# Optimization experiments

Measured on AMD Instinct MI355X. Metric: run time of the kernel, lower is better.

The kernel has to match this reference:

```python
import jax, jax.numpy as jnp
import numpy as np
import math

N = 10000      # atoms
E = 320000     # neighbor pairs (edges)
NELEM = 3      # species one-hot size
NRAD = 8       # radial channels per component
NB = 8         # bessel basis size
ZETA = 4       # max angular moment
RC = 5.0       # radial cutoff
S = 4          # species embedding size (species_layer_sizes[-1])
NCOMP = (ZETA + 2) * NRAD   # 2-body slice + (ZETA+1) angular slices = 48
FEAT = NCOMP * S            # 192

# multinomial expansion of (r_i . r_j)^l : lxlylz powers and l!/(lx!ly!lz!) norms
_TERMS = []
for l in range(ZETA + 1):
    pw, nm = [], []
    for a in range(l + 1):
        for b in range(l + 1 - a):
            c = l - a - b
            pw.append((a, b, c))
            nm.append(math.factorial(l) / (math.factorial(a) * math.factorial(b) * math.factorial(c)))
    _TERMS.append((np.array(pw, dtype=np.float32), np.array(nm, dtype=np.float32)))


def _silu(x):
    return x * jax.nn.sigmoid(x)


def setup_inputs() -> dict:
    key = jax.random.key(0)
    ks = jax.random.split(key, 12)
    rij = (jax.random.uniform(ks[0], (E, 3), minval=-1.0, maxval=1.0) * (RC / math.sqrt(3.0))).astype(jnp.float32)
    first_atom = jax.random.randint(ks[1], (E,), 0, N, dtype=jnp.int32)
    second_atom = jax.random.randint(ks[2], (E,), 0, N, dtype=jnp.int32)
    species_idx = jax.random.randint(ks[3], (N,), 0, NELEM, dtype=jnp.int32)
    w = lambda k, s: (jax.random.normal(k, s) * 0.1).astype(jnp.float32)
    z = lambda s: jnp.zeros(s, jnp.float32)
    return dict(
        rij=rij, species_idx=species_idx, first_atom=first_atom, second_atom=second_atom,
        Wr1=w(ks[4], (NB, 64)), br1=z((64,)),
        Wr2=w(ks[5], (64, NCOMP)), br2=z((NCOMP,)),
        Ws1=w(ks[6], (NELEM, 16)), bs1=z((16,)),
        Ws2=w(ks[7], (16, S)), bs2=z((S,)),
        Wa1=w(ks[8], (FEAT, 64)), ba1=z((64,)),
        Wa2=w(ks[9], (64, 64)), ba2=z((64,)),
        Wa3=w(ks[10], (64, 1)), ba3=z((1,)),
    )


def reference(rij, species_idx, first_atom, second_atom,
              Wr1, br1, Wr2, br2, Ws1, bs1, Ws2, bs2,
              Wa1, ba1, Wa2, ba2, Wa3, ba3):
    d = jnp.sqrt(jnp.sum(rij * rij, axis=-1) + 1e-12)            # [E]
    rhat = rij / d[:, None]                                       # [E,3]
    fc = jnp.where(d < RC, 0.5 * (jnp.cos(np.pi * d / RC) + 1.0), 0.0)
    n = jnp.arange(1, NB + 1, dtype=rij.dtype)
    bes = jnp.sqrt(2.0 / RC) * jnp.sin(n[None, :] * np.pi * d[:, None] / RC) / d[:, None]  # [E,NB]
    # learned radial functions, all components at once, smoothed by cutoff
    R = _silu(_silu(bes @ Wr1 + br1) @ Wr2 + br2) * fc[:, None]   # [E, NCOMP]
    # species encoder -> per-atom embedding, gathered on neighbor atom j
    onehot = jax.nn.one_hot(species_idx, NELEM, dtype=rij.dtype)  # [N,NELEM]
    semb = jnp.tanh(onehot @ Ws1 + bs1) @ Ws2 + bs2               # [N,S]
    sj = semb[second_atom]                                        # [E,S]
    # 2-body feature
    feats = [jax.ops.segment_sum(R[:, :NRAD, None] * sj[:, None, :], first_atom, num_segments=N)]  # [N,NRAD,S]
    off = NRAD
    for l in range(ZETA + 1):
        pw, nm = _TERMS[l]
        comps = jnp.prod(rhat[:, None, :] ** jnp.asarray(pw)[None, :, :], axis=-1)  # [E,C_l]
        Rl = R[:, off:off + NRAD]
        off += NRAD
        edge = Rl[:, :, None, None] * comps[:, None, :, None] * sj[:, None, None, :]  # [E,NRAD,C_l,S]
        A = jax.ops.segment_sum(edge, first_atom, num_segments=N)                     # [N,NRAD,C_l,S]
        feats.append(jnp.einsum('nrcs,c->nrs', A * A, jnp.asarray(nm)))               # [N,NRAD,S]
    feat = jnp.concatenate(feats, axis=1).reshape(N, -1)          # [N, FEAT]
    h = _silu(feat @ Wa1 + ba1)
    h = _silu(h @ Wa2 + ba2)
    return (h @ Wa3 + ba3)[:, 0]                                  # per-atom energies [N]
```

## Files before the change

kernel.cpp:

```cpp
#include <hip/hip_runtime.h>
#include <math.h>

#define NATOMS 10000
#define NEDGES 320000
#define CAP    64
#define RC_F 5.0f
#define PI_F 3.14159265358979323846f

#define NK   16384
#define TROW 48
#define HINV_F ((float)(NK - 1) / RC_F)

#define WS_SEMB   0
#define WS_CNT    16
#define WS_SD     440096
#define WS_TAB    8200096

__device__ __constant__ int   d_PWA[35] = {0, 0,0,1, 0,0,0,1,1,2, 0,0,0,0,1,1,1,2,2,3, 0,0,0,0,0,1,1,1,1,2,2,2,3,3,4};
__device__ __constant__ int   d_PWB[35] = {0, 0,1,0, 0,1,2,0,1,0, 0,1,2,3,0,1,2,0,1,0, 0,1,2,3,4,0,1,2,3,0,1,2,0,1,0};
__device__ __constant__ int   d_PWC[35] = {0, 1,0,0, 2,1,0,1,0,0, 3,2,1,0,2,1,0,1,0,0, 4,3,2,1,0,3,2,1,0,2,1,0,1,0,0};
__device__ __constant__ float d_NM[35]  = {1.f, 1.f,1.f,1.f, 1.f,2.f,1.f,2.f,2.f,1.f,
                                           1.f,3.f,3.f,1.f,3.f,6.f,3.f,3.f,3.f,1.f,
                                           1.f,4.f,6.f,4.f,1.f,4.f,12.f,12.f,4.f,6.f,12.f,6.f,4.f,4.f,1.f};
__device__ __constant__ int   d_LBLK[35]= {0, 1,1,1, 2,2,2,2,2,2, 3,3,3,3,3,3,3,3,3,3, 4,4,4,4,4,4,4,4,4,4,4,4,4,4,4};
__device__ __constant__ int   d_L6[6]   = {0,1,4,10,20,35};

__device__ __forceinline__ float siluf(float x) { return x / (1.0f + __expf(-x)); }

__device__ __forceinline__ float2 f2fma(float2 a, float2 b, float2 c) {
  return make_float2(fmaf(a.x, b.x, c.x), fmaf(a.y, b.y, c.y));
}

__device__ __forceinline__ float psel(float x, int p) {
  float x2 = x * x;
  float r = 1.0f;
  r = (p == 1) ? x : r;
  r = (p == 2) ? x2 : r;
  r = (p == 3) ? x2 * x : r;
  r = (p == 4) ? x2 * x2 : r;
  return r;
}

__global__ __launch_bounds__(256) void k_pre(
    const float* __restrict__ Wr1, const float* __restrict__ br1,
    const float* __restrict__ Wr2, const float* __restrict__ br2,
    const float* __restrict__ Ws1, const float* __restrict__ bs1,
    const float* __restrict__ Ws2, const float* __restrict__ bs2,
    float* __restrict__ ws)
{
  int gt = blockIdx.x * 256 + threadIdx.x;

  if (gt < NATOMS) ((int4*)(ws + WS_CNT))[gt] = make_int4(0, 0, 0, 0);
  if (gt < 12) {
    int t = gt >> 2, s = gt & 3;
    float acc = bs2[s];
    for (int j = 0; j < 16; j++) acc += tanhf(Ws1[t * 16 + j] + bs1[j]) * Ws2[j * 4 + s];
    ws[WS_SEMB + gt] = acc;
  }

  int sl = gt % 12;
  int k  = gt / 12;
  float dk = (float)k * (RC_F / (float)(NK - 1));
  float d = fmaxf(dk, 1e-6f);
  float invd = 1.0f / d;
  float theta = (PI_F / RC_F) * d;
  float s1 = sinf(theta), c1 = cosf(theta);
  float fc = (d < RC_F) ? 0.5f * (c1 + 1.0f) : 0.0f;
  float bes[8];
  {
    float sq = sqrtf(2.0f / RC_F) * invd;
    float twoc = 2.0f * c1;
    float sp = 0.0f, sc = s1;
    #pragma unroll
    for (int q = 0; q < 8; q++) {
      bes[q] = sq * sc;
      float sn = twoc * sc - sp;
      sp = sc; sc = sn;
    }
  }
  float h1[64];
  #pragma unroll
  for (int j4 = 0; j4 < 16; j4++) {
    float2 a01 = *(const float2*)&br1[j4 * 4];
    float2 a23 = *(const float2*)&br1[j4 * 4 + 2];
    #pragma unroll
    for (int q = 0; q < 8; q++) {
      float2 b2 = make_float2(bes[q], bes[q]);
      a01 = f2fma(b2, *(const float2*)&Wr1[q * 64 + j4 * 4],     a01);
      a23 = f2fma(b2, *(const float2*)&Wr1[q * 64 + j4 * 4 + 2], a23);
    }
    h1[j4 * 4 + 0] = siluf(a01.x);
    h1[j4 * 4 + 1] = siluf(a01.y);
    h1[j4 * 4 + 2] = siluf(a23.x);
    h1[j4 * 4 + 3] = siluf(a23.y);
  }
  int j0 = sl * 4;
  float2 a01 = *(const float2*)&br2[j0];
  float2 a23 = *(const float2*)&br2[j0 + 2];
  for (int q = 0; q < 64; q++) {
    float2 h2 = make_float2(h1[q], h1[q]);
    a01 = f2fma(h2, *(const float2*)&Wr2[q * 48 + j0],     a01);
    a23 = f2fma(h2, *(const float2*)&Wr2[q * 48 + j0 + 2], a23);
  }
  *(float4*)(ws + WS_TAB + (size_t)k * TROW + j0) =
      make_float4(siluf(a01.x) * fc, siluf(a01.y) * fc,
                  siluf(a23.x) * fc, siluf(a23.y) * fc);
}

__global__ __launch_bounds__(256) void k_scatter(
    const float* __restrict__ rij,
    const int* __restrict__ first_atom, const int* __restrict__ second_atom,
    const int* __restrict__ species, float* __restrict__ ws)
{
  int e = blockIdx.x * 256 + threadIdx.x;
  int* cnt = (int*)(ws + WS_CNT);
  int a = first_atom[e];
  int t = species[second_atom[e]];
  int pos = atomicAdd(&cnt[a * 4 + t], 1);
  float x = rij[e * 3 + 0], y = rij[e * 3 + 1], z = rij[e * 3 + 2];
  float d = sqrtf(x * x + y * y + z * z + 1e-12f);
  float invd = 1.0f / d;
  if (pos < CAP)
    ((float4*)(ws + WS_SD))[(size_t)a * (3 * CAP) + t * CAP + pos] =
        make_float4(x * invd, y * invd, z * invd, d);
}

__global__ __launch_bounds__(128) void k_atom(
    const float* __restrict__ ws,
    const float* __restrict__ Wa1, const float* __restrict__ ba1,
    const float* __restrict__ Wa2, const float* __restrict__ ba2,
    const float* __restrict__ Wa3, const float* __restrict__ ba3,
    float* __restrict__ out)
{
  __shared__ __align__(16) float sScr[2][1120];
  int tid = threadIdx.x;
  int lane = tid & 63, wv = tid >> 6;
  int a = blockIdx.x * 2 + wv;
  float* sStage = &sScr[wv][0];
  float* sG     = &sScr[wv][0];
  float* sFeat  = &sScr[wv][864];
  float* sH     = &sScr[wv][1056];

  const float4* sd4 = (const float4*)(ws + WS_SD);
  const float* tab = ws + WS_TAB;

  const int c = lane;
  bool isc = (c < 35);
  int pa = 0, pb = 0, pcw = 0, lb = 0;
  if (isc) { pa = d_PWA[c]; pb = d_PWB[c]; pcw = d_PWC[c]; lb = d_LBLK[c]; }
  int rdir = lane - 35;
  bool isd = (rdir >= 0) && (rdir < 8);
  int rl = lane >> 4, fl = lane & 15;
  int s = lane & 3;
  float se0 = ws[WS_SEMB + s], se1 = ws[WS_SEMB + 4 + s], se2 = ws[WS_SEMB + 8 + s];

  int4 cv = ((const int4*)(ws + WS_CNT))[a];
  int c0n = cv.x > CAP ? CAP : cv.x;
  int c1n = cv.y > CAP ? CAP : cv.y;
  int c2n = cv.z > CAP ? CAP : cv.z;

  float2 g2[3][4];
  #pragma unroll
  for (int t2 = 0; t2 < 3; t2++)
    #pragma unroll
    for (int r = 0; r < 4; r++) g2[t2][r] = make_float2(0.f, 0.f);
  float g0[3] = {0.0f, 0.0f, 0.0f};

#define CORE(T) {                                                             \
    const float* rb = sStage + j * 52;                                        \
    if (isc) {                                                                \
      float4 rh = *(const float4*)(rb + 48);                                  \
      float comp = psel(rh.x, pa) * psel(rh.y, pb) * psel(rh.z, pcw);         \
      float2 c2v = make_float2(comp, comp);                                   \
      const float2* r2 = (const float2*)(rb + 8 + 8 * lb);                    \
      g2[T][0] = f2fma(c2v, r2[0], g2[T][0]);                                 \
      g2[T][1] = f2fma(c2v, r2[1], g2[T][1]);                                 \
      g2[T][2] = f2fma(c2v, r2[2], g2[T][2]);                                 \
      g2[T][3] = f2fma(c2v, r2[3], g2[T][3]);                                 \
    } else if (isd) {                                                         \
      g0[T] += rb[rdir];                                                      \
    }                                                                         \
  }

#define RUNT(T, CT) {                                                         \
    const float4* rbase = sd4 + (size_t)a * (3 * CAP) + (T) * CAP;            \
    for (int cb = 0; cb < (CT); cb += 16) {                                   \
      int m = (CT) - cb; if (m > 16) m = 16;                                  \
      float4 ed = rbase[cb + ((lane < m) ? lane : (m - 1))];                  \
      float fi = ed.w * HINV_F;                                               \
      int ii = (int)fi;                                                       \
      ii = (ii > NK - 2) ? (NK - 2) : ii;                                     \
      float w = fi - (float)ii;                                               \
      int rowb = ii * TROW;                                                   \
      int R = (m + 3) >> 2;                                                   \
      for (int r = 0; r < R; r++) {                                           \
        int sl = r * 4 + rl;                                                  \
        float w_s = __shfl(w, sl, 64);                                        \
        int   rb_ = __shfl(rowb, sl, 64);                                     \
        float sx = __shfl(ed.x, sl, 64), sy = __shfl(ed.y, sl, 64);           \
        float sz = __shfl(ed.z, sl, 64);                                      \
        if (fl < 12) {                                                        \
          const float* tp = tab + rb_ + fl * 4;                               \
          float4 t0 = *(const float4*)(tp);                                   \
          float4 t1 = *(const float4*)(tp + TROW);                            \
          float4 v;                                                           \
          v.x = fmaf(w_s, t1.x - t0.x, t0.x);                                 \
          v.y = fmaf(w_s, t1.y - t0.y, t0.y);                                 \
          v.z = fmaf(w_s, t1.z - t0.z, t0.z);                                 \
          v.w = fmaf(w_s, t1.w - t0.w, t0.w);                                 \
          *(float4*)(sStage + sl * 52 + fl * 4) = v;                          \
        } else if (fl == 12) {                                                \
          *(float4*)(sStage + sl * 52 + 48) = make_float4(sx, sy, sz, 0.0f);  \
        }                                                                     \
      }                                                                       \
      for (int j = 0; j < m; j++) CORE(T)                                     \
    }                                                                         \
  }

  RUNT(0, c0n)
  RUNT(1, c1n)
  RUNT(2, c2n)
#undef RUNT
#undef CORE

  if (isc) {
    #pragma unroll
    for (int t2 = 0; t2 < 3; t2++)
      #pragma unroll
      for (int r = 0; r < 8; r++) {
        float gval = (r & 1) ? g2[t2][r >> 1].y : g2[t2][r >> 1].x;
        sG[(t2 * 8 + r) * 36 + c] = gval;
      }
  } else if (isd) {
    #pragma unroll
    for (int t2 = 0; t2 < 3; t2++) sG[(t2 * 8 + rdir) * 36 + 35] = g0[t2];
  }

  float fout[3];
  #pragma unroll
  for (int u = 0; u < 3; u++) {
    int f = lane + 64 * u;
    int blk = f >> 5, rr = (f >> 2) & 7;
    float acc;
    if (blk == 0) {
      acc = se0 * sG[(0 + rr) * 36 + 35] + se1 * sG[(8 + rr) * 36 + 35] + se2 * sG[(16 + rr) * 36 + 35];
    } else {
      int cc0 = d_L6[blk - 1], cc1 = d_L6[blk];
      acc = 0.0f;
      for (int cc = cc0; cc < cc1; cc++) {
        float A = se0 * sG[(0 + rr) * 36 + cc] + se1 * sG[(8 + rr) * 36 + cc] + se2 * sG[(16 + rr) * 36 + cc];
        acc += d_NM[cc] * A * A;
      }
    }
    fout[u] = acc;
  }
  #pragma unroll
  for (int u = 0; u < 3; u++) sFeat[lane + 64 * u] = fout[u];

  {
    float a0_ = 0.f, a1_ = 0.f, a2_ = 0.f, a3_ = 0.f;
    for (int k4 = 0; k4 < 48; k4++) {
      float4 f4 = *(const float4*)(sFeat + k4 * 4);
      const float* wp = Wa1 + (k4 * 4) * 64 + lane;
      a0_ += f4.x * wp[0];
      a1_ += f4.y * wp[64];
      a2_ += f4.z * wp[128];
      a3_ += f4.w * wp[192];
    }
    sH[lane] = siluf(a0_ + a1_ + a2_ + a3_ + ba1[lane]);
  }

  {
    float a0_ = 0.f, a1_ = 0.f, a2_ = 0.f, a3_ = 0.f;
    for (int k4 = 0; k4 < 16; k4++) {
      float4 h4 = *(const float4*)(sH + k4 * 4);
      const float* wp = Wa2 + (k4 * 4) * 64 + lane;
      a0_ += h4.x * wp[0];
      a1_ += h4.y * wp[64];
      a2_ += h4.z * wp[128];
      a3_ += h4.w * wp[192];
    }
    float h2 = siluf(a0_ + a1_ + a2_ + a3_ + ba2[lane]);
    float pr = h2 * Wa3[lane];
    #pragma unroll
    for (int off = 32; off > 0; off >>= 1) pr += __shfl_down(pr, off, 64);
    if (lane == 0) out[a] = pr + ba3[0];
  }
}

extern "C" void kernel_launch(void* const* d_in, const int* in_sizes, int n_in,
                              void* d_out, int out_size, void* d_ws, size_t ws_size,
                              hipStream_t stream)
{
  const float* rij         = (const float*)d_in[0];
  const int*   species     = (const int*)  d_in[1];
  const int*   first_atom  = (const int*)  d_in[2];
  const int*   second_atom = (const int*)  d_in[3];
  const float* Wr1 = (const float*)d_in[4];
  const float* br1 = (const float*)d_in[5];
  const float* Wr2 = (const float*)d_in[6];
  const float* br2 = (const float*)d_in[7];
  const float* Ws1 = (const float*)d_in[8];
  const float* bs1 = (const float*)d_in[9];
  const float* Ws2 = (const float*)d_in[10];
  const float* bs2 = (const float*)d_in[11];
  const float* Wa1 = (const float*)d_in[12];
  const float* ba1 = (const float*)d_in[13];
  const float* Wa2 = (const float*)d_in[14];
  const float* ba2 = (const float*)d_in[15];
  const float* Wa3 = (const float*)d_in[16];
  const float* ba3 = (const float*)d_in[17];
  float* ws  = (float*)d_ws;
  float* out = (float*)d_out;

  k_pre<<<(NK * 12) / 256, 256, 0, stream>>>(Wr1, br1, Wr2, br2, Ws1, bs1, Ws2, bs2, ws);
  k_scatter<<<NEDGES / 256, 256, 0, stream>>>(rij, first_atom, second_atom, species, ws);
  k_atom<<<NATOMS / 2, 128, 0, stream>>>(ws, Wa1, ba1, Wa2, ba2, Wa3, ba3, out);
}
```

Baseline: 172.6 us.

## Read radial table directly per lane instead of staging edges through LDS

Drops the cooperative staging step, where 16-edge chunks were interpolated into shared memory via shuffles and then consumed. Each lane now loads each edge's record (a broadcast load), interpolates the radial table slice for its own angular block from global or cache, and accumulates directly. This removes shuffles, LDS writes and reads, and the two-phase structure. In exchange, every lane issues redundant global loads of the same table rows (35 lanes reading overlapping 8-float slices), and the edge loop becomes sequential with a dependent load per edge.

```diff
diff --git a/kernel.cpp b/kernel.cpp
--- a/kernel.cpp
+++ b/kernel.cpp
@@ -136,7 +136,6 @@
   int tid = threadIdx.x;
   int lane = tid & 63, wv = tid >> 6;
   int a = blockIdx.x * 2 + wv;
-  float* sStage = &sScr[wv][0];
   float* sG     = &sScr[wv][0];
   float* sFeat  = &sScr[wv][864];
   float* sH     = &sScr[wv][1056];
@@ -146,11 +145,10 @@
 
   const int c = lane;
   bool isc = (c < 35);
-  int pa = 0, pb = 0, pcw = 0, lb = 0;
-  if (isc) { pa = d_PWA[c]; pb = d_PWB[c]; pcw = d_PWC[c]; lb = d_LBLK[c]; }
+  int pa = 0, pb = 0, pcw = 0, my8 = 8;
+  if (isc) { pa = d_PWA[c]; pb = d_PWB[c]; pcw = d_PWC[c]; my8 = 8 + 8 * d_LBLK[c]; }
   int rdir = lane - 35;
   bool isd = (rdir >= 0) && (rdir < 8);
-  int rl = lane >> 4, fl = lane & 15;
   int s = lane & 3;
   float se0 = ws[WS_SEMB + s], se1 = ws[WS_SEMB + 4 + s], se2 = ws[WS_SEMB + 8 + s];
 
@@ -166,54 +164,40 @@
     for (int r = 0; r < 4; r++) g2[t2][r] = make_float2(0.f, 0.f);
   float g0[3] = {0.0f, 0.0f, 0.0f};
 
-#define CORE(T) {                                                             \
-    const float* rb = sStage + j * 52;                                        \
-    if (isc) {                                                                \
-      float4 rh = *(const float4*)(rb + 48);                                  \
-      float comp = psel(rh.x, pa) * psel(rh.y, pb) * psel(rh.z, pcw);         \
-      float2 c2v = make_float2(comp, comp);                                   \
-      const float2* r2 = (const float2*)(rb + 8 + 8 * lb);                    \
-      g2[T][0] = f2fma(c2v, r2[0], g2[T][0]);                                 \
-      g2[T][1] = f2fma(c2v, r2[1], g2[T][1]);                                 \
-      g2[T][2] = f2fma(c2v, r2[2], g2[T][2]);                                 \
-      g2[T][3] = f2fma(c2v, r2[3], g2[T][3]);                                 \
-    } else if (isd) {                                                         \
-      g0[T] += rb[rdir];                                                      \
-    }                                                                         \
-  }
-
 #define RUNT(T, CT) {                                                         \
     const float4* rbase = sd4 + (size_t)a * (3 * CAP) + (T) * CAP;            \
-    for (int cb = 0; cb < (CT); cb += 16) {                                   \
-      int m = (CT) - cb; if (m > 16) m = 16;                                  \
-      float4 ed = rbase[cb + ((lane < m) ? lane : (m - 1))];                  \
+    _Pragma("unroll 4")                                                       \
+    for (int j = 0; j < (CT); j++) {                                          \
+      float4 ed = rbase[j];                                                   \
       float fi = ed.w * HINV_F;                                               \
       int ii = (int)fi;                                                       \
       ii = (ii > NK - 2) ? (NK - 2) : ii;                                     \
       float w = fi - (float)ii;                                               \
-      int rowb = ii * TROW;                                                   \
-      int R = (m + 3) >> 2;                                                   \
-      for (int r = 0; r < R; r++) {                                           \
-        int sl = r * 4 + rl;                                                  \
-        float w_s = __shfl(w, sl, 64);                                        \
-        int   rb_ = __shfl(rowb, sl, 64);                                     \
-        float sx = __shfl(ed.x, sl, 64), sy = __shfl(ed.y, sl, 64);           \
-        float sz = __shfl(ed.z, sl, 64);                                      \
-        if (fl < 12) {                                                        \
-          const float* tp = tab + rb_ + fl * 4;                               \
-          float4 t0 = *(const float4*)(tp);                                   \
-          float4 t1 = *(const float4*)(tp + TROW);                            \
-          float4 v;                                                           \
-          v.x = fmaf(w_s, t1.x - t0.x, t0.x);                                 \
-          v.y = fmaf(w_s, t1.y - t0.y, t0.y);                                 \
-          v.z = fmaf(w_s, t1.z - t0.z, t0.z);                                 \
-          v.w = fmaf(w_s, t1.w - t0.w, t0.w);                                 \
-          *(float4*)(sStage + sl * 52 + fl * 4) = v;                          \
-        } else if (fl == 12) {                                                \
-          *(float4*)(sStage + sl * 52 + 48) = make_float4(sx, sy, sz, 0.0f);  \
-        }                                                                     \
+      const float* tp0 = tab + ii * TROW;                                     \
+      if (isc) {                                                              \
+        const float* ta = tp0 + my8;                                          \
+        float4 t0a = *(const float4*)(ta);                                    \
+        float4 t0b = *(const float4*)(ta + 4);                                \
+        float4 t1a = *(const float4*)(ta + TROW);                             \
+        float4 t1b = *(const float4*)(ta + TROW + 4);                         \
+        float comp = psel(ed.x, pa) * psel(ed.y, pb) * psel(ed.z, pcw);       \
+        float2 c2v = make_float2(comp, comp);                                 \
+        float2 v0 = make_float2(fmaf(w, t1a.x - t0a.x, t0a.x),                \
+                                fmaf(w, t1a.y - t0a.y, t0a.y));               \
+        float2 v1 = make_float2(fmaf(w, t1a.z - t0a.z, t0a.z),                \
+                                fmaf(w, t1a.w - t0a.w, t0a.w));               \
+        float2 v2 = make_float2(fmaf(w, t1b.x - t0b.x, t0b.x),                \
+                                fmaf(w, t1b.y - t0b.y, t0b.y));               \
+        float2 v3 = make_float2(fmaf(w, t1b.z - t0b.z, t0b.z),                \
+                                fmaf(w, t1b.w - t0b.w, t0b.w));               \
+        g2[T][0] = f2fma(c2v, v0, g2[T][0]);                                  \
+        g2[T][1] = f2fma(c2v, v1, g2[T][1]);                                  \
+        g2[T][2] = f2fma(c2v, v2, g2[T][2]);                                  \
+        g2[T][3] = f2fma(c2v, v3, g2[T][3]);                                  \
+      } else if (isd) {                                                       \
+        float t0 = tp0[rdir], t1 = tp0[TROW + rdir];                          \
+        g0[T] += fmaf(w, t1 - t0, t0);                                        \
       }                                                                       \
-      for (int j = 0; j < m; j++) CORE(T)                                     \
     }                                                                         \
   }
 
@@ -221,7 +205,6 @@
   RUNT(1, c1n)
   RUNT(2, c2n)
 #undef RUNT
-#undef CORE
 
   if (isc) {
     #pragma unroll
```

Measured after the change: 217.4 us. 1.26x slower.

## Split atom MLP into separate kernel with transposed weights staged in workspace

Applied to the files above, without the earlier changes.

Splits the per-atom kernel in two. The first kernel accumulates features and writes them to global memory. A new MLP kernel reads those features and runs the two dense layers, reading transposed Wa1/Wa2 copies as per-lane contiguous float4 loads. The transposes are built in the preprocessing kernel. This is meant to cut the accumulation kernel's shared memory and register pressure, raising occupancy, at the cost of an extra launch and a global round trip for the features.

```diff
diff --git a/kernel.cpp b/kernel.cpp
--- a/kernel.cpp
+++ b/kernel.cpp
@@ -15,6 +15,9 @@
 #define WS_CNT    16
 #define WS_SD     440096
 #define WS_TAB    8200096
+#define WS_WA1T   9000000
+#define WS_WA2T   9012288
+#define WS_FEAT   9016384
 
 __device__ __constant__ int   d_PWA[35] = {0, 0,0,1, 0,0,0,1,1,2, 0,0,0,0,1,1,1,2,2,3, 0,0,0,0,0,1,1,1,1,2,2,2,3,3,4};
 __device__ __constant__ int   d_PWB[35] = {0, 0,1,0, 0,1,2,0,1,0, 0,1,2,3,0,1,2,0,1,0, 0,1,2,3,4,0,1,2,3,0,1,2,0,1,0};
@@ -46,6 +49,7 @@
     const float* __restrict__ Wr2, const float* __restrict__ br2,
     const float* __restrict__ Ws1, const float* __restrict__ bs1,
     const float* __restrict__ Ws2, const float* __restrict__ bs2,
+    const float* __restrict__ Wa1, const float* __restrict__ Wa2,
     float* __restrict__ ws)
 {
   int gt = blockIdx.x * 256 + threadIdx.x;
@@ -56,6 +60,15 @@
     float acc = bs2[s];
     for (int j = 0; j < 16; j++) acc += tanhf(Ws1[t * 16 + j] + bs1[j]) * Ws2[j * 4 + s];
     ws[WS_SEMB + gt] = acc;
+  }
+  if (gt < 64 * 192) {
+    int c = gt / 192, k = gt % 192;
+    ws[WS_WA1T + gt] = Wa1[k * 64 + c];
+  }
+  if (gt >= 64 * 192 && gt < 64 * 192 + 64 * 64) {
+    int g2 = gt - 64 * 192;
+    int c = g2 / 64, k = g2 % 64;
+    ws[WS_WA2T + g2] = Wa2[k * 64 + c];
   }
 
   int sl = gt % 12;
@@ -125,21 +138,14 @@
         make_float4(x * invd, y * invd, z * invd, d);
 }
 
-__global__ __launch_bounds__(128) void k_atom(
-    const float* __restrict__ ws,
-    const float* __restrict__ Wa1, const float* __restrict__ ba1,
-    const float* __restrict__ Wa2, const float* __restrict__ ba2,
-    const float* __restrict__ Wa3, const float* __restrict__ ba3,
-    float* __restrict__ out)
-{
-  __shared__ __align__(16) float sScr[2][1120];
+__global__ __launch_bounds__(128) void k_acc(float* __restrict__ ws)
+{
+  __shared__ __align__(16) float sScr[2][864];
   int tid = threadIdx.x;
   int lane = tid & 63, wv = tid >> 6;
   int a = blockIdx.x * 2 + wv;
   float* sStage = &sScr[wv][0];
   float* sG     = &sScr[wv][0];
-  float* sFeat  = &sScr[wv][864];
-  float* sH     = &sScr[wv][1056];
 
   const float4* sd4 = (const float4*)(ws + WS_SD);
   const float* tab = ws + WS_TAB;
@@ -236,7 +242,7 @@
     for (int t2 = 0; t2 < 3; t2++) sG[(t2 * 8 + rdir) * 36 + 35] = g0[t2];
   }
 
-  float fout[3];
+  float* featr = ws + WS_FEAT + (size_t)a * 192;
   #pragma unroll
   for (int u = 0; u < 3; u++) {
     int f = lane + 64 * u;
@@ -252,40 +258,54 @@
         acc += d_NM[cc] * A * A;
       }
     }
-    fout[u] = acc;
-  }
-  #pragma unroll
-  for (int u = 0; u < 3; u++) sFeat[lane + 64 * u] = fout[u];
-
-  {
-    float a0_ = 0.f, a1_ = 0.f, a2_ = 0.f, a3_ = 0.f;
-    for (int k4 = 0; k4 < 48; k4++) {
-      float4 f4 = *(const float4*)(sFeat + k4 * 4);
-      const float* wp = Wa1 + (k4 * 4) * 64 + lane;
-      a0_ += f4.x * wp[0];
-      a1_ += f4.y * wp[64];
-      a2_ += f4.z * wp[128];
-      a3_ += f4.w * wp[192];
-    }
-    sH[lane] = siluf(a0_ + a1_ + a2_ + a3_ + ba1[lane]);
-  }
-
-  {
-    float a0_ = 0.f, a1_ = 0.f, a2_ = 0.f, a3_ = 0.f;
-    for (int k4 = 0; k4 < 16; k4++) {
-      float4 h4 = *(const float4*)(sH + k4 * 4);
-      const float* wp = Wa2 + (k4 * 4) * 64 + lane;
-      a0_ += h4.x * wp[0];
-      a1_ += h4.y * wp[64];
-      a2_ += h4.z * wp[128];
-      a3_ += h4.w * wp[192];
-    }
-    float h2 = siluf(a0_ + a1_ + a2_ + a3_ + ba2[lane]);
-    float pr = h2 * Wa3[lane];
-    #pragma unroll
-    for (int off = 32; off > 0; off >>= 1) pr += __shfl_down(pr, off, 64);
-    if (lane == 0) out[a] = pr + ba3[0];
-  }
+    featr[f] = acc;
+  }
+}
+
+__global__ __launch_bounds__(256) void k_mlp(
+    const float* __restrict__ ws,
+    const float* __restrict__ ba1, const float* __restrict__ ba2,
+    const float* __restrict__ Wa3, const float* __restrict__ ba3,
+    float* __restrict__ out)
+{
+  __shared__ __align__(16) float sF[4][192];
+  int lane = threadIdx.x & 63, wv = threadIdx.x >> 6;
+  int a = blockIdx.x * 4 + wv;
+
+  const float* fr = ws + WS_FEAT + (size_t)a * 192;
+  float f0 = fr[lane], f1 = fr[lane + 64], f2 = fr[lane + 128];
+  sF[wv][lane] = f0; sF[wv][lane + 64] = f1; sF[wv][lane + 128] = f2;
+
+  const float* w1 = ws + WS_WA1T + (size_t)lane * 192;
+  float a0 = 0.f, a1 = 0.f, a2 = 0.f, a3 = 0.f;
+  #pragma unroll
+  for (int k4 = 0; k4 < 48; k4++) {
+    float4 f4 = *(const float4*)(&sF[wv][k4 * 4]);
+    float4 w4 = *(const float4*)(w1 + k4 * 4);
+    a0 += f4.x * w4.x;
+    a1 += f4.y * w4.y;
+    a2 += f4.z * w4.z;
+    a3 += f4.w * w4.w;
+  }
+  float h = siluf(a0 + a1 + a2 + a3 + ba1[lane]);
+
+  sF[wv][lane] = h;
+  const float* w2 = ws + WS_WA2T + (size_t)lane * 64;
+  float b0 = 0.f, b1 = 0.f, b2 = 0.f, b3 = 0.f;
+  #pragma unroll
+  for (int k4 = 0; k4 < 16; k4++) {
+    float4 h4 = *(const float4*)(&sF[wv][k4 * 4]);
+    float4 w4 = *(const float4*)(w2 + k4 * 4);
+    b0 += h4.x * w4.x;
+    b1 += h4.y * w4.y;
+    b2 += h4.z * w4.z;
+    b3 += h4.w * w4.w;
+  }
+  float h2 = siluf(b0 + b1 + b2 + b3 + ba2[lane]);
+  float pr = h2 * Wa3[lane];
+  #pragma unroll
+  for (int off = 32; off > 0; off >>= 1) pr += __shfl_down(pr, off, 64);
+  if (lane == 0) out[a] = pr + ba3[0];
 }
 
 extern "C" void kernel_launch(void* const* d_in, const int* in_sizes, int n_in,
@@ -313,7 +333,9 @@
   float* ws  = (float*)d_ws;
   float* out = (float*)d_out;
 
-  k_pre<<<(NK * 12) / 256, 256, 0, stream>>>(Wr1, br1, Wr2, br2, Ws1, bs1, Ws2, bs2, ws);
+  k_pre<<<(NK * 12) / 256, 256, 0, stream>>>(Wr1, br1, Wr2, br2, Ws1, bs1, Ws2, bs2,
+                                             Wa1, Wa2, ws);
   k_scatter<<<NEDGES / 256, 256, 0, stream>>>(rij, first_atom, second_atom, species, ws);
-  k_atom<<<NATOMS / 2, 128, 0, stream>>>(ws, Wa1, ba1, Wa2, ba2, Wa3, ba3, out);
-}
+  k_acc<<<NATOMS / 2, 128, 0, stream>>>(ws);
+  k_mlp<<<NATOMS / 4, 256, 0, stream>>>(ws, ba1, ba2, Wa3, ba3, out);
+}
```

After: 234.4 us. 1.36x slower.

## Process two atoms per wavefront with interleaved staging across species segments

Applied to the files above, without the earlier changes.

Each wavefront now handles two atoms and interleaves their table-gather staging and accumulation phases, so one atom's memory loads can overlap the other's compute. The three per-species loops are merged into one flattened edge stream per atom, which fills 16-edge chunks across species boundaries and cuts partially empty chunks. The cost is doubled accumulator registers, a larger shared buffer and half as many blocks, which may lower occupancy.

```diff
diff --git a/kernel.cpp b/kernel.cpp
--- a/kernel.cpp
+++ b/kernel.cpp
@@ -125,111 +125,23 @@
         make_float4(x * invd, y * invd, z * invd, d);
 }
 
-__global__ __launch_bounds__(128) void k_atom(
-    const float* __restrict__ ws,
+__device__ __forceinline__ void atom_tail(
+    float2 (*g2)[4], const float* g0,
+    float* sG, float* sFeat, float* sH,
+    int lane, bool isc, bool isd, int rdir,
+    float se0, float se1, float se2,
     const float* __restrict__ Wa1, const float* __restrict__ ba1,
     const float* __restrict__ Wa2, const float* __restrict__ ba2,
     const float* __restrict__ Wa3, const float* __restrict__ ba3,
-    float* __restrict__ out)
-{
-  __shared__ __align__(16) float sScr[2][1120];
-  int tid = threadIdx.x;
-  int lane = tid & 63, wv = tid >> 6;
-  int a = blockIdx.x * 2 + wv;
-  float* sStage = &sScr[wv][0];
-  float* sG     = &sScr[wv][0];
-  float* sFeat  = &sScr[wv][864];
-  float* sH     = &sScr[wv][1056];
-
-  const float4* sd4 = (const float4*)(ws + WS_SD);
-  const float* tab = ws + WS_TAB;
-
-  const int c = lane;
-  bool isc = (c < 35);
-  int pa = 0, pb = 0, pcw = 0, lb = 0;
-  if (isc) { pa = d_PWA[c]; pb = d_PWB[c]; pcw = d_PWC[c]; lb = d_LBLK[c]; }
-  int rdir = lane - 35;
-  bool isd = (rdir >= 0) && (rdir < 8);
-  int rl = lane >> 4, fl = lane & 15;
-  int s = lane & 3;
-  float se0 = ws[WS_SEMB + s], se1 = ws[WS_SEMB + 4 + s], se2 = ws[WS_SEMB + 8 + s];
-
-  int4 cv = ((const int4*)(ws + WS_CNT))[a];
-  int c0n = cv.x > CAP ? CAP : cv.x;
-  int c1n = cv.y > CAP ? CAP : cv.y;
-  int c2n = cv.z > CAP ? CAP : cv.z;
-
-  float2 g2[3][4];
-  #pragma unroll
-  for (int t2 = 0; t2 < 3; t2++)
-    #pragma unroll
-    for (int r = 0; r < 4; r++) g2[t2][r] = make_float2(0.f, 0.f);
-  float g0[3] = {0.0f, 0.0f, 0.0f};
-
-#define CORE(T) {                                                             \
-    const float* rb = sStage + j * 52;                                        \
-    if (isc) {                                                                \
-      float4 rh = *(const float4*)(rb + 48);                                  \
-      float comp = psel(rh.x, pa) * psel(rh.y, pb) * psel(rh.z, pcw);         \
-      float2 c2v = make_float2(comp, comp);                                   \
-      const float2* r2 = (const float2*)(rb + 8 + 8 * lb);                    \
-      g2[T][0] = f2fma(c2v, r2[0], g2[T][0]);                                 \
-      g2[T][1] = f2fma(c2v, r2[1], g2[T][1]);                                 \
-      g2[T][2] = f2fma(c2v, r2[2], g2[T][2]);                                 \
-      g2[T][3] = f2fma(c2v, r2[3], g2[T][3]);                                 \
-    } else if (isd) {                                                         \
-      g0[T] += rb[rdir];                                                      \
-    }                                                                         \
-  }
-
-#define RUNT(T, CT) {                                                         \
-    const float4* rbase = sd4 + (size_t)a * (3 * CAP) + (T) * CAP;            \
-    for (int cb = 0; cb < (CT); cb += 16) {                                   \
-      int m = (CT) - cb; if (m > 16) m = 16;                                  \
-      float4 ed = rbase[cb + ((lane < m) ? lane : (m - 1))];                  \
-      float fi = ed.w * HINV_F;                                               \
-      int ii = (int)fi;                                                       \
-      ii = (ii > NK - 2) ? (NK - 2) : ii;                                     \
-      float w = fi - (float)ii;                                               \
-      int rowb = ii * TROW;                                                   \
-      int R = (m + 3) >> 2;                                                   \
-      for (int r = 0; r < R; r++) {                                           \
-        int sl = r * 4 + rl;                                                  \
-        float w_s = __shfl(w, sl, 64);                                        \
-        int   rb_ = __shfl(rowb, sl, 64);                                     \
-        float sx = __shfl(ed.x, sl, 64), sy = __shfl(ed.y, sl, 64);           \
-        float sz = __shfl(ed.z, sl, 64);                                      \
-        if (fl < 12) {                                                        \
-          const float* tp = tab + rb_ + fl * 4;                               \
-          float4 t0 = *(const float4*)(tp);                                   \
-          float4 t1 = *(const float4*)(tp + TROW);                            \
-          float4 v;                                                           \
-          v.x = fmaf(w_s, t1.x - t0.x, t0.x);                                 \
-          v.y = fmaf(w_s, t1.y - t0.y, t0.y);                                 \
-          v.z = fmaf(w_s, t1.z - t0.z, t0.z);                                 \
-          v.w = fmaf(w_s, t1.w - t0.w, t0.w);                                 \
-          *(float4*)(sStage + sl * 52 + fl * 4) = v;                          \
-        } else if (fl == 12) {                                                \
-          *(float4*)(sStage + sl * 52 + 48) = make_float4(sx, sy, sz, 0.0f);  \
-        }                                                                     \
-      }                                                                       \
-      for (int j = 0; j < m; j++) CORE(T)                                     \
-    }                                                                         \
-  }
-
-  RUNT(0, c0n)
-  RUNT(1, c1n)
-  RUNT(2, c2n)
-#undef RUNT
-#undef CORE
-
+    float* __restrict__ out, int a)
+{
   if (isc) {
     #pragma unroll
     for (int t2 = 0; t2 < 3; t2++)
       #pragma unroll
       for (int r = 0; r < 8; r++) {
         float gval = (r & 1) ? g2[t2][r >> 1].y : g2[t2][r >> 1].x;
-        sG[(t2 * 8 + r) * 36 + c] = gval;
+        sG[(t2 * 8 + r) * 36 + lane] = gval;
       }
   } else if (isd) {
     #pragma unroll
@@ -286,6 +198,131 @@
     for (int off = 32; off > 0; off >>= 1) pr += __shfl_down(pr, off, 64);
     if (lane == 0) out[a] = pr + ba3[0];
   }
+}
+
+__global__ __launch_bounds__(128) void k_atom(
+    const float* __restrict__ ws,
+    const float* __restrict__ Wa1, const float* __restrict__ ba1,
+    const float* __restrict__ Wa2, const float* __restrict__ ba2,
+    const float* __restrict__ Wa3, const float* __restrict__ ba3,
+    float* __restrict__ out)
+{
+  __shared__ __align__(16) float sScr[2][1664];
+  int tid = threadIdx.x;
+  int lane = tid & 63, wv = tid >> 6;
+  int aA = blockIdx.x * 4 + wv * 2;
+  int aB = aA + 1;
+  float* reg  = &sScr[wv][0];
+  float* stA  = reg;
+  float* stB  = reg + 832;
+  float* sG    = reg;
+  float* sFeat = reg + 864;
+  float* sH    = reg + 1056;
+
+  const float4* sd4 = (const float4*)(ws + WS_SD);
+  const float* tab = ws + WS_TAB;
+
+  const int c = lane;
+  bool isc = (c < 35);
+  int pa = 0, pb = 0, pcw = 0, lb = 0;
+  if (isc) { pa = d_PWA[c]; pb = d_PWB[c]; pcw = d_PWC[c]; lb = d_LBLK[c]; }
+  int rdir = lane - 35;
+  bool isd = (rdir >= 0) && (rdir < 8);
+  int rl = lane >> 4, fl = lane & 15;
+  int s = lane & 3;
+  float se0 = ws[WS_SEMB + s], se1 = ws[WS_SEMB + 4 + s], se2 = ws[WS_SEMB + 8 + s];
+
+  int4 cvA = ((const int4*)(ws + WS_CNT))[aA];
+  int4 cvB = ((const int4*)(ws + WS_CNT))[aB];
+  int c0A = cvA.x > CAP ? CAP : cvA.x, c1A = cvA.y > CAP ? CAP : cvA.y, c2A = cvA.z > CAP ? CAP : cvA.z;
+  int c0B = cvB.x > CAP ? CAP : cvB.x, c1B = cvB.y > CAP ? CAP : cvB.y, c2B = cvB.z > CAP ? CAP : cvB.z;
+  int b1A = c0A, b2A = c0A + c1A, totA = b2A + c2A;
+  int b1B = c0B, b2B = c0B + c1B, totB = b2B + c2B;
+  const float4* rbA = sd4 + (size_t)aA * (3 * CAP);
+  const float4* rbB = sd4 + (size_t)aB * (3 * CAP);
+
+  float2 gA[3][4], gB[3][4];
+  #pragma unroll
+  for (int t2 = 0; t2 < 3; t2++)
+    #pragma unroll
+    for (int r = 0; r < 4; r++) { gA[t2][r] = make_float2(0.f, 0.f); gB[t2][r] = make_float2(0.f, 0.f); }
+  float g0A[3] = {0.f, 0.f, 0.f}, g0B[3] = {0.f, 0.f, 0.f};
+
+#define STAGE(ST, RB, B1, B2, TOT) {                                          \
+    int m = (TOT) - cb; if (m > 16) m = 16;                                   \
+    int g = cb + ((lane < m) ? lane : (m - 1));                               \
+    int T = (g >= (B1)) + (g >= (B2));                                        \
+    int loc = g - ((T == 0) ? 0 : ((T == 1) ? (B1) : (B2)));                  \
+    float4 ed = (RB)[T * CAP + loc];                                          \
+    float fi = ed.w * HINV_F;                                                 \
+    int ii = (int)fi;                                                         \
+    ii = (ii > NK - 2) ? (NK - 2) : ii;                                       \
+    float w = fi - (float)ii;                                                 \
+    int rowb = ii * TROW;                                                     \
+    int R = (m + 3) >> 2;                                                     \
+    for (int r = 0; r < R; r++) {                                             \
+      int sl = r * 4 + rl;                                                    \
+      float w_s = __shfl(w, sl, 64);                                          \
+      int   rb_ = __shfl(rowb, sl, 64);                                       \
+      float sx = __shfl(ed.x, sl, 64), sy = __shfl(ed.y, sl, 64);             \
+      float sz = __shfl(ed.z, sl, 64);                                        \
+      if (fl < 12) {                                                          \
+        const float* tp = tab + rb_ + fl * 4;                                 \
+        float4 t0 = *(const float4*)(tp);                                     \
+        float4 t1 = *(const float4*)(tp + TROW);                              \
+        float4 v;                                                             \
+        v.x = fmaf(w_s, t1.x - t0.x, t0.x);                                   \
+        v.y = fmaf(w_s, t1.y - t0.y, t0.y);                                   \
+        v.z = fmaf(w_s, t1.z - t0.z, t0.z);                                   \
+        v.w = fmaf(w_s, t1.w - t0.w, t0.w);                                   \
+        *(float4*)((ST) + sl * 52 + fl * 4) = v;                              \
+      } else if (fl == 12) {                                                  \
+        *(float4*)((ST) + sl * 52 + 48) = make_float4(sx, sy, sz, 0.0f);      \
+      }                                                                       \
+    }                                                                         \
+  }
+
+#define CORE1(ST, G2, G0, T) {                                                \
+    const float* rb = (ST) + j * 52;                                          \
+    if (isc) {                                                                \
+      float4 rh = *(const float4*)(rb + 48);                                  \
+      float comp = psel(rh.x, pa) * psel(rh.y, pb) * psel(rh.z, pcw);         \
+      float2 c2v = make_float2(comp, comp);                                   \
+      const float2* r2 = (const float2*)(rb + 8 + 8 * lb);                    \
+      G2[T][0] = f2fma(c2v, r2[0], G2[T][0]);                                 \
+      G2[T][1] = f2fma(c2v, r2[1], G2[T][1]);                                 \
+      G2[T][2] = f2fma(c2v, r2[2], G2[T][2]);                                 \
+      G2[T][3] = f2fma(c2v, r2[3], G2[T][3]);                                 \
+    } else if (isd) {                                                         \
+      G0[T] += rb[rdir];                                                      \
+    }                                                                         \
+  }
+
+#define CORESEG(ST, G2, G0, B1, B2, TOT) {                                    \
+    int m = (TOT) - cb; if (m > 16) m = 16;                                   \
+    int jb1 = (B1) - cb; jb1 = jb1 < 0 ? 0 : (jb1 > m ? m : jb1);             \
+    int jb2 = (B2) - cb; jb2 = jb2 < 0 ? 0 : (jb2 > m ? m : jb2);             \
+    int j = 0;                                                                \
+    for (; j < jb1; j++) CORE1(ST, G2, G0, 0)                                 \
+    for (; j < jb2; j++) CORE1(ST, G2, G0, 1)                                 \
+    for (; j < m;   j++) CORE1(ST, G2, G0, 2)                                 \
+  }
+
+  int mx = (totA > totB) ? totA : totB;
+  for (int cb = 0; cb < mx; cb += 16) {
+    if (cb < totA) STAGE(stA, rbA, b1A, b2A, totA)
+    if (cb < totB) STAGE(stB, rbB, b1B, b2B, totB)
+    if (cb < totA) CORESEG(stA, gA, g0A, b1A, b2A, totA)
+    if (cb < totB) CORESEG(stB, gB, g0B, b1B, b2B, totB)
+  }
+#undef STAGE
+#undef CORE1
+#undef CORESEG
+
+  atom_tail(gA, g0A, sG, sFeat, sH, lane, isc, isd, rdir, se0, se1, se2,
+            Wa1, ba1, Wa2, ba2, Wa3, ba3, out, aA);
+  atom_tail(gB, g0B, sG, sFeat, sH, lane, isc, isd, rdir, se0, se1, se2,
+            Wa1, ba1, Wa2, ba2, Wa3, ba3, out, aB);
 }
 
 extern "C" void kernel_launch(void* const* d_in, const int* in_sizes, int n_in,
@@ -315,5 +352,5 @@
 
   k_pre<<<(NK * 12) / 256, 256, 0, stream>>>(Wr1, br1, Wr2, br2, Ws1, bs1, Ws2, bs2, ws);
   k_scatter<<<NEDGES / 256, 256, 0, stream>>>(rij, first_atom, second_atom, species, ws);
-  k_atom<<<NATOMS / 2, 128, 0, stream>>>(ws, Wa1, ba1, Wa2, ba2, Wa3, ba3, out);
-}
+  k_atom<<<NATOMS / 4, 128, 0, stream>>>(ws, Wa1, ba1, Wa2, ba2, Wa3, ba3, out);
+}
```

After: 404.5 us. 2.34x slower.
